# Optimization experiments

Measured on AMD Instinct MI355X. Metric: run time of the kernel, lower is better.

Reference implementation:

```python
import jax, jax.numpy as jnp
import numpy as np

KS = 2        # kernel_size
DIL = 1       # dilation
FILTERS = 512
Z_DIM = 128
B, C, T = 8, 512, 4096
TZ = T + 2 * (KS - 1)


def _conv1d(x, w, b):
    # x: (B, L, Cin), w: (ks, Cin, Cout) -> VALID conv, channels-last (keras Conv1D)
    y = jax.lax.conv_general_dilated(x, w, window_strides=(1,), padding='VALID',
                                     dimension_numbers=('NWC', 'WIO', 'NWC'))
    return y + b


def _adaptor(z, w1, b1, w2, b2):
    return _conv1d(jax.nn.relu(_conv1d(z, w1, b1)), w2, b2)


def setup_inputs() -> dict:
    key = jax.random.key(0)
    ks = jax.random.split(key, 10)
    lim = np.sqrt(6.0 / FILTERS)
    u = lambda k, shp: jax.random.uniform(k, shp, jnp.float32, -lim, lim)
    return {
        'x': jax.random.normal(ks[0], (B, C, T), jnp.float32),
        'z': jax.random.normal(ks[1], (B, TZ, Z_DIM), jnp.float32),
        'ww1': u(ks[2], (KS, Z_DIM, FILTERS)), 'wb1': jnp.zeros((FILTERS,), jnp.float32),
        'ww2': u(ks[3], (KS, FILTERS, FILTERS)), 'wb2': jnp.zeros((FILTERS,), jnp.float32),
        'bw1': u(ks[4], (KS, Z_DIM, FILTERS)), 'bb1': jnp.zeros((FILTERS,), jnp.float32),
        'bw2': u(ks[5], (KS, FILTERS, FILTERS)), 'bb2': jnp.zeros((FILTERS,), jnp.float32),
    }


def reference(x, z, ww1, wb1, ww2, wb2, bw1, bb1, bw2, bb2):
    m = x.shape[1]
    t = x.shape[2]
    pad = DIL * (KS - 1)
    xp = jnp.pad(x, ((0, 0), (0, 0), (0, pad)))
    end = t + pad
    # im2col-style unfold: (B, C*KS, T)
    xu = jnp.concatenate([xp[:, :, pad - i * DIL: end - i * DIL] for i in range(KS)], axis=1)
    weights = _adaptor(z, ww1, wb1, ww2, wb2)   # (B, T, F)
    bias = _adaptor(z, bw1, bb1, bw2, bb2)      # (B, T, F)
    y = jnp.matmul(xu, weights)                 # (B, C*KS, F)
    return y[:, :m, :] + bias[:, :m, :]
```

## Files before the change

kernel.cpp:

```cpp
#include <hip/hip_runtime.h>

typedef short short8 __attribute__((ext_vector_type(8)));
typedef float float4v __attribute__((ext_vector_type(4)));
typedef __attribute__((address_space(1))) const unsigned int gu32;
typedef __attribute__((address_space(3))) unsigned int lu32;

__device__ __forceinline__ unsigned short f2bf(float f) {
  unsigned int u = __builtin_bit_cast(unsigned int, f);
  u += 0x7FFFu + ((u >> 16) & 1u);
  return (unsigned short)(u >> 16);
}
__device__ __forceinline__ float bf2f(unsigned short s) {
  return __builtin_bit_cast(float, (unsigned int)s << 16);
}

__global__ __launch_bounds__(256) void prep_fused(
    const float* __restrict__ x,
    const float* __restrict__ z,
    const float* __restrict__ ww1, const float* __restrict__ ww2,
    const float* __restrict__ bw1, const float* __restrict__ bw2,
    unsigned short* __restrict__ xs, unsigned short* __restrict__ xz,
    float* __restrict__ rs,
    unsigned short* __restrict__ w1T, unsigned short* __restrict__ w2T,
    unsigned short* __restrict__ b1T, unsigned short* __restrict__ b2T,
    unsigned short* __restrict__ zb)
{
  if (blockIdx.x < 4096) {
    __shared__ float red[4];
    long long r = blockIdx.x;
    const float* xr = x + r * 4096;
    int t0 = threadIdx.x * 16;
    float v[17];
    const float4* xr4 = (const float4*)(xr + t0);
#pragma unroll
    for (int q = 0; q < 4; ++q) {
      float4 f = xr4[q];
      v[q * 4] = f.x; v[q * 4 + 1] = f.y; v[q * 4 + 2] = f.z; v[q * 4 + 3] = f.w;
    }
    v[16] = (t0 + 16 < 4096) ? xr[t0 + 16] : 0.f;
    unsigned int spk[8], zpk[8];
    float sum = 0.f;
#pragma unroll
    for (int q = 0; q < 8; ++q) {
      unsigned short s0 = f2bf(v[2 * q + 1]);
      unsigned short s1 = f2bf(v[2 * q + 2]);
      sum += bf2f(s0);
      sum += bf2f(s1);
      spk[q] = (unsigned int)s0 | ((unsigned int)s1 << 16);
      unsigned short z0 = (t0 == 0 && q == 0) ? (unsigned short)0 : f2bf(v[2 * q]);
      unsigned short z1 = f2bf(v[2 * q + 1]);
      zpk[q] = (unsigned int)z0 | ((unsigned int)z1 << 16);
    }
    *(uint4*)(xs + r * 4096 + t0)     = *(uint4*)(spk);
    *(uint4*)(xs + r * 4096 + t0 + 8) = *(uint4*)(spk + 4);
    *(uint4*)(xz + r * 4096 + t0)     = *(uint4*)(zpk);
    *(uint4*)(xz + r * 4096 + t0 + 8) = *(uint4*)(zpk + 4);
#pragma unroll
    for (int off = 32; off > 0; off >>= 1) sum += __shfl_down(sum, off);
    if ((threadIdx.x & 63) == 0) red[threadIdx.x >> 6] = sum;
    __syncthreads();
    if (threadIdx.x == 0) rs[r] = red[0] + red[1] + red[2] + red[3];
  } else {
    int i = (blockIdx.x - 4096) * 256 + threadIdx.x;
    if (i < 131072) {
      int n = i & 511, k = i >> 9;
      w1T[n * 256 + k] = f2bf(ww1[i]);
    } else if (i < 655360) {
      int j = i - 131072; int n = j & 511, k = j >> 9;
      w2T[n * 1024 + k] = f2bf(ww2[j]);
    } else if (i < 786432) {
      int j = i - 655360; int n = j & 511, k = j >> 9;
      b1T[n * 256 + k] = f2bf(bw1[j]);
    } else if (i < 1310720) {
      int j = i - 786432; int n = j & 511, k = j >> 9;
      b2T[n * 1024 + k] = f2bf(bw2[j]);
    } else {
      int j = i - 1310720;
      zb[j] = f2bf(z[j]);
    }
  }
}

template<int BM, int BN, bool RELU, bool OBF16, bool TRANS, bool SPLITK>
__global__ __launch_bounds__(256)
void gemm_bt(const unsigned short* __restrict__ A,
             const unsigned short* __restrict__ A2,
             const unsigned short* __restrict__ Bt,
             const float* __restrict__ biasv,
             void* __restrict__ outp,
             void* __restrict__ outp2,
             int M, int Kchunk, int RPB, int EXTRA, int BSCALE,
             int nHalf, int bRowMask,
             long long bStrideB, long long outBatchStride, int outLd)
{
  constexpr int WM = BM / 2, WN = BN / 2;
  constexpr int NI = WM / 16, NJ = WN / 16;
  constexpr int AI = BM / 64;
  constexpr int BI = BN / 64;
  constexpr int SA1 = BM * 32, SB1 = BN * 32;
  constexpr int STAGE = 2 * SA1 + 2 * SB1;
  constexpr int SMEMN = TRANS ? ((128 * 136 > STAGE) ? 128 * 136 : STAGE) : STAGE;
  __shared__ unsigned short smem[SMEMN];

  const int tid  = threadIdx.x;
  const int lane = tid & 63;
  const int wave = tid >> 6;
  const int wm = wave >> 1, wn = wave & 1;
  const int lr = lane & 15, quad = lane >> 4;

  const int r0 = blockIdx.x * BM;
  const int n0 = blockIdx.y * BN;
  const int bb = r0 / RPB;
  const int Ktot = SPLITK ? Kchunk * gridDim.z : Kchunk;
  const int kOff = SPLITK ? blockIdx.z * Kchunk : 0;
  const long long bOffB = (long long)bb * bStrideB;
  const unsigned short* Ae = (nHalf && n0 >= nHalf) ? A2 : A;

  const int srow = lane >> 2;
  const int sg = (lane & 3) ^ (srow & 3);
  const unsigned short* gA[AI]; unsigned short* ldsA[AI];
#pragma unroll
  for (int c = 0; c < AI; ++c) {
    int instr = c * 4 + wave;
    int row = instr * 16 + srow;
    int r = r0 + row; if (r > M - 1) r = M - 1;
    gA[c] = Ae + ((long long)r + (long long)(r / RPB) * EXTRA) * BSCALE + kOff + sg * 8;
    ldsA[c] = smem + instr * 512;
  }
  const unsigned short* gB[BI]; unsigned short* ldsB[BI];
#pragma unroll
  for (int c = 0; c < BI; ++c) {
    int instr = c * 4 + wave;
    int row = instr * 16 + srow;
    gB[c] = Bt + (long long)((n0 + row) & bRowMask) * Ktot + bOffB + kOff + sg * 8;
    ldsB[c] = smem + 2 * SA1 + instr * 512;
  }

  int aoff[NI], boff[NJ];
#pragma unroll
  for (int i = 0; i < NI; ++i) {
    int rr = wm * WM + i * 16 + lr;
    aoff[i] = rr * 32 + ((quad ^ (rr & 3)) * 8);
  }
#pragma unroll
  for (int j = 0; j < NJ; ++j) {
    int rr = wn * WN + j * 16 + lr;
    boff[j] = 2 * SA1 + rr * 32 + ((quad ^ (rr & 3)) * 8);
  }

  float4v acc[NI][NJ];
  const float4v z4 = {0.f, 0.f, 0.f, 0.f};
#pragma unroll
  for (int i = 0; i < NI; ++i)
#pragma unroll
    for (int j = 0; j < NJ; ++j) acc[i][j] = z4;

  for (int k0 = 0; k0 < Kchunk; k0 += 64) {
#pragma unroll
    for (int h = 0; h < 2; ++h) {
#pragma unroll
      for (int c = 0; c < AI; ++c)
        __builtin_amdgcn_global_load_lds((gu32*)(gA[c] + k0 + h * 32),
                                         (lu32*)(ldsA[c] + h * SA1), 16, 0, 0);
#pragma unroll
      for (int c = 0; c < BI; ++c)
        __builtin_amdgcn_global_load_lds((gu32*)(gB[c] + k0 + h * 32),
                                         (lu32*)(ldsB[c] + h * SB1), 16, 0, 0);
    }
    __syncthreads();
#pragma unroll
    for (int h = 0; h < 2; ++h) {
      short8 af[NI], bfr[NJ];
#pragma unroll
      for (int i = 0; i < NI; ++i) af[i] = *(const short8*)(smem + h * SA1 + aoff[i]);
#pragma unroll
      for (int j = 0; j < NJ; ++j) bfr[j] = *(const short8*)(smem + h * SB1 + boff[j]);
#pragma unroll
      for (int i = 0; i < NI; ++i)
#pragma unroll
        for (int j = 0; j < NJ; ++j)
          acc[i][j] = __builtin_amdgcn_mfma_f32_16x16x32_bf16(af[i], bfr[j], acc[i][j], 0, 0, 0);
    }
    __syncthreads();
  }

  if (TRANS) {
    unsigned short* Ts = smem;
#pragma unroll
    for (int j = 0; j < NJ; ++j) {
      int fr = wn * WN + j * 16 + lr;
      float bv = biasv[n0 + fr];
#pragma unroll
      for (int i = 0; i < NI; ++i) {
        int tr = wm * WM + i * 16 + quad * 4;
        unsigned long long pk = 0;
#pragma unroll
        for (int g = 0; g < 4; ++g) {
          float vv = acc[i][j][g] + bv;
          if (RELU) vv = fmaxf(vv, 0.f);
          pk |= (unsigned long long)f2bf(vv) << (16 * g);
        }
        *(unsigned long long*)(Ts + fr * 136 + tr) = pk;
      }
    }
    __syncthreads();
    int fr = tid >> 1, sgg = tid & 1;
    int t0l = r0 - bb * RPB;
    unsigned short* dst = (unsigned short*)outp + (long long)bb * outBatchStride
                        + (long long)(n0 + fr) * outLd + t0l + sgg * 64;
    const unsigned short* srcp = Ts + fr * 136 + sgg * 64;
#pragma unroll
    for (int u = 0; u < 8; ++u)
      *(uint4*)(dst + u * 8) = *(const uint4*)(srcp + u * 8);
  } else {
    void* op = (SPLITK && blockIdx.z) ? outp2 : outp;
#pragma unroll
    for (int j = 0; j < NJ; ++j) {
      int n_g = n0 + wn * WN + j * 16 + lr;
      float bv = biasv ? biasv[n_g] : 0.f;
#pragma unroll
      for (int i = 0; i < NI; ++i) {
        int r_base = r0 + wm * WM + i * 16 + quad * 4;
#pragma unroll
        for (int g = 0; g < 4; ++g) {
          int r_g = r_base + g;
          if (r_g >= M) continue;
          float v = acc[i][j][g] + bv;
          if (RELU) v = fmaxf(v, 0.f);
          long long oidx = (long long)r_g * outLd + n_g;
          if (OBF16) ((unsigned short*)op)[oidx] = f2bf(v);
          else       ((float*)op)[oidx] = v;
        }
      }
    }
  }
}

__global__ __launch_bounds__(256) void final_gemm3(
    const unsigned short* __restrict__ p0,
    const unsigned short* __restrict__ p1,
    const unsigned short* __restrict__ h1b,
    const unsigned short* __restrict__ w2T,
    const unsigned short* __restrict__ b2T,
    const float* __restrict__ rs,
    const float* __restrict__ wb2,
    const float* __restrict__ bb2,
    float* __restrict__ out)
{
  constexpr int SA1 = 64 * 32, SB1 = 64 * 32;
  __shared__ unsigned short smem[2 * SA1 + 2 * SB1];
  const int tid = threadIdx.x;
  const int lane = tid & 63, wave = tid >> 6;
  const int wm = wave >> 1, wn = wave & 1;
  const int lr = lane & 15, quad = lane >> 4;
  const int r0 = blockIdx.x * 64, n0 = blockIdx.y * 64;

  const int srow = lane >> 2;
  const int sg = (lane & 3) ^ (srow & 3);
  const int row = wave * 16 + srow;
  const int rA = r0 + row;
  const int rB = n0 + row;
  const unsigned short* aP[3] = {
    p0 + (long long)rA * 1024 + sg * 8,
    p1 + (long long)rA * 1024 + sg * 8,
    h1b + ((long long)rA + (rA >> 9)) * 512 + sg * 8 };
  const unsigned short* bP[3] = {
    w2T + (long long)rB * 1024 + sg * 8,
    w2T + (long long)rB * 1024 + sg * 8,
    b2T + (long long)rB * 1024 + sg * 8 };
  unsigned short* ldsA = smem + wave * 512;
  unsigned short* ldsB = smem + 2 * SA1 + wave * 512;

  int aoff[2], boff[2];
#pragma unroll
  for (int i = 0; i < 2; ++i) {
    int rr = wm * 32 + i * 16 + lr;
    aoff[i] = rr * 32 + ((quad ^ (rr & 3)) * 8);
    int nn = wn * 32 + i * 16 + lr;
    boff[i] = 2 * SA1 + nn * 32 + ((quad ^ (nn & 3)) * 8);
  }

  float4v acc[2][2];
  const float4v z4 = {0.f, 0.f, 0.f, 0.f};
  acc[0][0] = z4; acc[0][1] = z4; acc[1][0] = z4; acc[1][1] = z4;

  for (int k0 = 0; k0 < 3072; k0 += 64) {
    int seg = k0 >> 10;
    int kk = k0 & 1023;
#pragma unroll
    for (int h = 0; h < 2; ++h) {
      __builtin_amdgcn_global_load_lds((gu32*)(aP[seg] + kk + h * 32),
                                       (lu32*)(ldsA + h * SA1), 16, 0, 0);
      __builtin_amdgcn_global_load_lds((gu32*)(bP[seg] + kk + h * 32),
                                       (lu32*)(ldsB + h * SB1), 16, 0, 0);
    }
    __syncthreads();
#pragma unroll
    for (int h = 0; h < 2; ++h) {
      short8 af[2], bfr[2];
      af[0] = *(const short8*)(smem + h * SA1 + aoff[0]);
      af[1] = *(const short8*)(smem + h * SA1 + aoff[1]);
      bfr[0] = *(const short8*)(smem + h * SB1 + boff[0]);
      bfr[1] = *(const short8*)(smem + h * SB1 + boff[1]);
#pragma unroll
      for (int i = 0; i < 2; ++i)
#pragma unroll
        for (int j = 0; j < 2; ++j)
          acc[i][j] = __builtin_amdgcn_mfma_f32_16x16x32_bf16(af[i], bfr[j], acc[i][j], 0, 0, 0);
    }
    __syncthreads();
  }

#pragma unroll
  for (int j = 0; j < 2; ++j) {
    int n_g = n0 + wn * 32 + j * 16 + lr;
    float w2b = wb2[n_g], bbv = bb2[n_g];
#pragma unroll
    for (int i = 0; i < 2; ++i) {
      int rb = r0 + wm * 32 + i * 16 + quad * 4;
#pragma unroll
      for (int g = 0; g < 4; ++g) {
        int r_g = rb + g;
        out[(long long)r_g * 512 + n_g] = acc[i][j][g] + rs[r_g] * w2b + bbv;
      }
    }
  }
}

extern "C" void kernel_launch(void* const* d_in, const int* in_sizes, int n_in,
                              void* d_out, int out_size, void* d_ws, size_t ws_size,
                              hipStream_t stream) {
  const float* x   = (const float*)d_in[0];
  const float* z   = (const float*)d_in[1];
  const float* ww1 = (const float*)d_in[2];
  const float* wb1 = (const float*)d_in[3];
  const float* ww2 = (const float*)d_in[4];
  const float* wb2 = (const float*)d_in[5];
  const float* bw1 = (const float*)d_in[6];
  const float* bb1 = (const float*)d_in[7];
  const float* bw2 = (const float*)d_in[8];
  const float* bb2 = (const float*)d_in[9];

  char* ws = (char*)d_ws;
  unsigned short* xs  = (unsigned short*)ws; ws += 16777216ll * 2;
  unsigned short* xz  = (unsigned short*)ws; ws += 16777216ll * 2;
  unsigned short* zb  = (unsigned short*)ws; ws += 4196352ll  * 2;
  unsigned short* h1T = (unsigned short*)ws; ws += 16777216ll * 2;
  unsigned short* h1b = (unsigned short*)ws; ws += 2101248ll  * 2;
  unsigned short* w2T = (unsigned short*)ws; ws += 524288ll * 2;
  unsigned short* b2T = (unsigned short*)ws; ws += 524288ll * 2;
  float* rs = (float*)ws;                    ws += 4096ll * 4;
  char* tail = ws;
  unsigned short* w1T = (unsigned short*)tail;
  unsigned short* b1T = (unsigned short*)tail + 131072;
  unsigned short* p0  = zb;
  unsigned short* p1  = (unsigned short*)tail;

  prep_fused<<<4096 + 21512, 256, 0, stream>>>(
      x, z, ww1, ww2, bw1, bw2, xs, xz, rs, w1T, w2T, b1T, b2T, zb);

  gemm_bt<128, 128, true, true, true, false><<<dim3(256, 4), 256, 0, stream>>>(
      zb, nullptr, w1T, wb1, h1T, nullptr,
      32768, 256, 4096, 2, 128, 0, 0xFFFF, 0, 512ll * 4096, 4096);
  gemm_bt<64, 128, true, true, false, false><<<dim3(65, 4), 256, 0, stream>>>(
      zb, nullptr, b1T, bb1, h1b, nullptr,
      4104, 256, 513, 3585, 128, 0, 0xFFFF, 0, 0, 512);
  gemm_bt<128, 128, false, true, false, true><<<dim3(32, 8, 2), 256, 0, stream>>>(
      xs, xz, h1T, nullptr, p0, p1,
      4096, 2048, 512, 0, 4096, 512, 511, 512ll * 4096, 0, 1024);
  final_gemm3<<<dim3(64, 8), 256, 0, stream>>>(
      p0, p1, h1b, w2T, b2T, rs, wb2, bb2, (float*)d_out);
}
```

Before: 286.3 us.

## Split big GEMM four ways along K, add reduce kernel, deepen first GEMM stage

The large x-by-h1 GEMM now splits K into four chunks when the workspace has room, giving 1024 blocks instead of 512. A new reduce kernel sums the bf16 partials into one buffer, so final_gemm3 reads one summed A operand instead of two and its K loop shrinks from 3072 to 2048. The first adaptor GEMM also loads four 32-wide K slices per stage instead of two, halving its barriers. The cost is an extra kernel launch, extra partial-sum traffic, and an extra bf16 rounding step in the reduction.

```diff
diff --git a/kernel.cpp b/kernel.cpp
--- a/kernel.cpp
+++ b/kernel.cpp
@@ -81,7 +81,31 @@
   }
 }
 
-template<int BM, int BN, bool RELU, bool OBF16, bool TRANS, bool SPLITK>
+__global__ __launch_bounds__(256) void reduce_p(
+    unsigned short* __restrict__ p0, const unsigned short* __restrict__ p1,
+    const unsigned short* __restrict__ p2, const unsigned short* __restrict__ p3,
+    int nz)
+{
+  long long i = (long long)(blockIdx.x * 256 + threadIdx.x) * 8;
+  short8 a0 = *(const short8*)(p0 + i);
+  short8 a1 = *(const short8*)(p1 + i);
+  unsigned short st[8];
+  if (nz == 4) {
+    short8 a2 = *(const short8*)(p2 + i);
+    short8 a3 = *(const short8*)(p3 + i);
+#pragma unroll
+    for (int j = 0; j < 8; ++j)
+      st[j] = f2bf((bf2f((unsigned short)a0[j]) + bf2f((unsigned short)a1[j]))
+                 + (bf2f((unsigned short)a2[j]) + bf2f((unsigned short)a3[j])));
+  } else {
+#pragma unroll
+    for (int j = 0; j < 8; ++j)
+      st[j] = f2bf(bf2f((unsigned short)a0[j]) + bf2f((unsigned short)a1[j]));
+  }
+  *(uint4*)(p0 + i) = *(const uint4*)(st);
+}
+
+template<int BM, int BN, bool RELU, bool OBF16, bool TRANS, bool SPLITK, int NH>
 __global__ __launch_bounds__(256)
 void gemm_bt(const unsigned short* __restrict__ A,
              const unsigned short* __restrict__ A2,
@@ -89,6 +113,8 @@
              const float* __restrict__ biasv,
              void* __restrict__ outp,
              void* __restrict__ outp2,
+             void* __restrict__ pc,
+             void* __restrict__ pd,
              int M, int Kchunk, int RPB, int EXTRA, int BSCALE,
              int nHalf, int bRowMask,
              long long bStrideB, long long outBatchStride, int outLd)
@@ -98,9 +124,10 @@
   constexpr int AI = BM / 64;
   constexpr int BI = BN / 64;
   constexpr int SA1 = BM * 32, SB1 = BN * 32;
-  constexpr int STAGE = 2 * SA1 + 2 * SB1;
+  constexpr int STAGE = NH * (SA1 + SB1);
   constexpr int SMEMN = TRANS ? ((128 * 136 > STAGE) ? 128 * 136 : STAGE) : STAGE;
   __shared__ unsigned short smem[SMEMN];
+  unsigned short* sB0 = smem + NH * SA1;
 
   const int tid  = threadIdx.x;
   const int lane = tid & 63;
@@ -133,7 +160,7 @@
     int instr = c * 4 + wave;
     int row = instr * 16 + srow;
     gB[c] = Bt + (long long)((n0 + row) & bRowMask) * Ktot + bOffB + kOff + sg * 8;
-    ldsB[c] = smem + 2 * SA1 + instr * 512;
+    ldsB[c] = sB0 + instr * 512;
   }
 
   int aoff[NI], boff[NJ];
@@ -145,7 +172,7 @@
 #pragma unroll
   for (int j = 0; j < NJ; ++j) {
     int rr = wn * WN + j * 16 + lr;
-    boff[j] = 2 * SA1 + rr * 32 + ((quad ^ (rr & 3)) * 8);
+    boff[j] = rr * 32 + ((quad ^ (rr & 3)) * 8);
   }
 
   float4v acc[NI][NJ];
@@ -155,9 +182,9 @@
 #pragma unroll
     for (int j = 0; j < NJ; ++j) acc[i][j] = z4;
 
-  for (int k0 = 0; k0 < Kchunk; k0 += 64) {
-#pragma unroll
-    for (int h = 0; h < 2; ++h) {
+  for (int k0 = 0; k0 < Kchunk; k0 += 32 * NH) {
+#pragma unroll
+    for (int h = 0; h < NH; ++h) {
 #pragma unroll
       for (int c = 0; c < AI; ++c)
         __builtin_amdgcn_global_load_lds((gu32*)(gA[c] + k0 + h * 32),
@@ -169,12 +196,12 @@
     }
     __syncthreads();
 #pragma unroll
-    for (int h = 0; h < 2; ++h) {
+    for (int h = 0; h < NH; ++h) {
       short8 af[NI], bfr[NJ];
 #pragma unroll
       for (int i = 0; i < NI; ++i) af[i] = *(const short8*)(smem + h * SA1 + aoff[i]);
 #pragma unroll
-      for (int j = 0; j < NJ; ++j) bfr[j] = *(const short8*)(smem + h * SB1 + boff[j]);
+      for (int j = 0; j < NJ; ++j) bfr[j] = *(const short8*)(sB0 + h * SB1 + boff[j]);
 #pragma unroll
       for (int i = 0; i < NI; ++i)
 #pragma unroll
@@ -213,7 +240,11 @@
     for (int u = 0; u < 8; ++u)
       *(uint4*)(dst + u * 8) = *(const uint4*)(srcp + u * 8);
   } else {
-    void* op = (SPLITK && blockIdx.z) ? outp2 : outp;
+    void* op = outp;
+    if (SPLITK) {
+      int zz = blockIdx.z;
+      op = (zz == 0) ? outp : (zz == 1) ? outp2 : (zz == 2) ? pc : pd;
+    }
 #pragma unroll
     for (int j = 0; j < NJ; ++j) {
       int n_g = n0 + wn * WN + j * 16 + lr;
@@ -237,8 +268,7 @@
 }
 
 __global__ __launch_bounds__(256) void final_gemm3(
-    const unsigned short* __restrict__ p0,
-    const unsigned short* __restrict__ p1,
+    const unsigned short* __restrict__ Gsum,
     const unsigned short* __restrict__ h1b,
     const unsigned short* __restrict__ w2T,
     const unsigned short* __restrict__ b2T,
@@ -260,12 +290,10 @@
   const int row = wave * 16 + srow;
   const int rA = r0 + row;
   const int rB = n0 + row;
-  const unsigned short* aP[3] = {
-    p0 + (long long)rA * 1024 + sg * 8,
-    p1 + (long long)rA * 1024 + sg * 8,
+  const unsigned short* aP[2] = {
+    Gsum + (long long)rA * 1024 + sg * 8,
     h1b + ((long long)rA + (rA >> 9)) * 512 + sg * 8 };
-  const unsigned short* bP[3] = {
-    w2T + (long long)rB * 1024 + sg * 8,
+  const unsigned short* bP[2] = {
     w2T + (long long)rB * 1024 + sg * 8,
     b2T + (long long)rB * 1024 + sg * 8 };
   unsigned short* ldsA = smem + wave * 512;
@@ -284,7 +312,7 @@
   const float4v z4 = {0.f, 0.f, 0.f, 0.f};
   acc[0][0] = z4; acc[0][1] = z4; acc[1][0] = z4; acc[1][1] = z4;
 
-  for (int k0 = 0; k0 < 3072; k0 += 64) {
+  for (int k0 = 0; k0 < 2048; k0 += 64) {
     int seg = k0 >> 10;
     int kk = k0 & 1023;
 #pragma unroll
@@ -355,19 +383,25 @@
   unsigned short* b1T = (unsigned short*)tail + 131072;
   unsigned short* p0  = zb;
   unsigned short* p1  = (unsigned short*)tail;
+  unsigned short* p2  = (unsigned short*)(tail + 8388608);
+  unsigned short* p3  = (unsigned short*)(tail + 16777216);
+
+  size_t fixed = (size_t)(tail - (char*)d_ws);
+  int nz = (ws_size >= fixed + 3ull * 8388608) ? 4 : 2;
 
   prep_fused<<<4096 + 21512, 256, 0, stream>>>(
       x, z, ww1, ww2, bw1, bw2, xs, xz, rs, w1T, w2T, b1T, b2T, zb);
 
-  gemm_bt<128, 128, true, true, true, false><<<dim3(256, 4), 256, 0, stream>>>(
-      zb, nullptr, w1T, wb1, h1T, nullptr,
+  gemm_bt<128, 128, true, true, true, false, 4><<<dim3(256, 4), 256, 0, stream>>>(
+      zb, nullptr, w1T, wb1, h1T, nullptr, nullptr, nullptr,
       32768, 256, 4096, 2, 128, 0, 0xFFFF, 0, 512ll * 4096, 4096);
-  gemm_bt<64, 128, true, true, false, false><<<dim3(65, 4), 256, 0, stream>>>(
-      zb, nullptr, b1T, bb1, h1b, nullptr,
+  gemm_bt<64, 128, true, true, false, false, 2><<<dim3(65, 4), 256, 0, stream>>>(
+      zb, nullptr, b1T, bb1, h1b, nullptr, nullptr, nullptr,
       4104, 256, 513, 3585, 128, 0, 0xFFFF, 0, 0, 512);
-  gemm_bt<128, 128, false, true, false, true><<<dim3(32, 8, 2), 256, 0, stream>>>(
-      xs, xz, h1T, nullptr, p0, p1,
-      4096, 2048, 512, 0, 4096, 512, 511, 512ll * 4096, 0, 1024);
+  gemm_bt<128, 128, false, true, false, true, 2><<<dim3(32, 8, nz), 256, 0, stream>>>(
+      xs, xz, h1T, nullptr, p0, p1, p2, p3,
+      4096, 4096 / nz, 512, 0, 4096, 512, 511, 512ll * 4096, 0, 1024);
+  reduce_p<<<2048, 256, 0, stream>>>(p0, p1, p2, p3, nz);
   final_gemm3<<<dim3(64, 8), 256, 0, stream>>>(
-      p0, p1, h1b, w2T, b2T, rs, wb2, bb2, (float*)d_out);
-}
+      p0, h1b, w2T, b2T, rs, wb2, bb2, (float*)d_out);
+}
```

New measurement: 294.6 us. 1.03x slower.
